# Kernel optimization log

Measured on AMD Instinct MI355X. Metric: run time of the kernel, lower is better.

## Reference

```python
import jax, jax.numpy as jnp
import numpy as np

NEAR, FAR, N_SAMPLES = 1.0, 6.0, 64
FAR_APPEND = 1000.0


def setup_inputs() -> dict:
    key = jax.random.key(0)
    ks = jax.random.split(key, 8)
    B, R = 2, 4096
    # pixel coords in a 128x128 image
    x_pix = jax.random.uniform(ks[0], (B, R, 2), dtype=jnp.float32) * 128.0
    # plausible pinhole intrinsics (fx=fy=128, cx=cy=64)
    K = jnp.array([[128.0, 0.0, 64.0], [0.0, 128.0, 64.0], [0.0, 0.0, 1.0]], dtype=jnp.float32)
    intrinsics = jnp.tile(K[None], (B, 1, 1))
    # identity rotation, small translation cam2world
    c2w = jnp.eye(4, dtype=jnp.float32).at[:3, 3].set(jnp.array([0.1, -0.2, 0.5]))
    cam2world = jnp.tile(c2w[None], (B, 1, 1))
    H = 256
    W1 = jax.random.normal(ks[1], (3, H), dtype=jnp.float32) / np.sqrt(3.0)
    b1 = jnp.zeros((H,), jnp.float32)
    W2 = jax.random.normal(ks[2], (H, H), dtype=jnp.float32) / np.sqrt(H)
    b2 = jnp.zeros((H,), jnp.float32)
    W3 = jax.random.normal(ks[3], (H, 4), dtype=jnp.float32) / np.sqrt(H)
    b3 = jnp.zeros((4,), jnp.float32)
    return {"x_pix": x_pix, "intrinsics": intrinsics, "cam2world": cam2world,
            "W1": W1, "b1": b1, "W2": W2, "b2": b2, "W3": W3, "b3": b3}


def _radiance_field(pts, W1, b1, W2, b2, W3, b3):
    # pts: (B, N, 3) -> sigma (B, N, 1), rad (B, N, 3)
    h = jax.nn.relu(pts @ W1 + b1)
    h = jax.nn.relu(h @ W2 + b2)
    o = h @ W3 + b3
    return jax.nn.relu(o[..., :1]), jax.nn.sigmoid(o[..., 1:])


def _get_world_rays(x_pix, intrinsics, cam2world):
    B, R, _ = x_pix.shape
    inv_K = jnp.linalg.inv(intrinsics)  # (B,3,3)
    xy_hom = jnp.concatenate([x_pix, jnp.ones((B, R, 1), x_pix.dtype)], axis=-1)  # (B,R,3)
    dirs_cam = jnp.einsum("bij,brj->bri", inv_K, xy_hom)  # unnormalized cam-frame dirs
    dirs_hom = jnp.concatenate([dirs_cam, jnp.zeros((B, R, 1), x_pix.dtype)], axis=-1)  # w=0 vector
    dirs_world = jnp.einsum("bij,brj->bri", cam2world, dirs_hom)[..., :3]
    origins = jnp.broadcast_to(cam2world[:, None, :3, 3], (B, R, 3))
    return origins, dirs_world


def _volume_integral(z_vals, sigmas, radiances):
    # z_vals: (S,); sigmas: (B,R,S,1); radiances: (B,R,S,3)
    dists = jnp.diff(z_vals, append=jnp.array([FAR_APPEND], z_vals.dtype))  # (S,)
    alpha = 1.0 - jnp.exp(-sigmas * dists[None, None, :, None])  # (B,R,S,1)
    Ts = jnp.cumprod(1.0 - alpha, axis=2)  # inclusive cumprod, matching torch
    weights = alpha * Ts  # (B,R,S,1)
    rgb = jnp.sum(weights * radiances, axis=2)  # (B,R,3)
    depth_map = jnp.einsum("brsv,s->brv", weights, z_vals)  # (B,R,1)
    return rgb, depth_map, weights


def reference(x_pix, intrinsics, cam2world, W1, b1, W2, b2, W3, b3):
    B, R = x_pix.shape[0], x_pix.shape[1]
    ros, rds = _get_world_rays(x_pix, intrinsics, cam2world)
    z_vals = jnp.linspace(NEAR, FAR, N_SAMPLES, dtype=x_pix.dtype)  # (S,)
    pts = ros[:, :, None, :] + rds[:, :, None, :] * z_vals[None, None, :, None]  # (B,R,S,3)
    pts = pts.reshape(B, -1, 3)
    sigma, rad = _radiance_field(pts, W1, b1, W2, b2, W3, b3)
    sigma = sigma.reshape(B, R, N_SAMPLES, 1)
    rad = rad.reshape(B, R, N_SAMPLES, 3)
    rgb, depth_map, weights = _volume_integral(z_vals, sigma, rad)
    accum = jnp.sum(weights, axis=-2)  # (B,R,1)
    rgb = rgb + (1.0 - accum)  # white background
    return rgb, depth_map
```

## Files before the change

kernel.cpp:

```cpp
#include <hip/hip_runtime.h>

typedef unsigned short u16;
typedef _Float16 f16x8 __attribute__((ext_vector_type(8)));
typedef float    f32x4  __attribute__((ext_vector_type(4)));
typedef float    f32x16 __attribute__((ext_vector_type(16)));

#define NRAYS 8192

#define WS_W2T  0
#define WS_B2   131072
#define WS_W3   132096
#define WS_B3   136192
#define WS_W1   136208
#define WS_B1   139280
#define WS_INTR 140304
#define WS_C2W  140384

__device__ __forceinline__ float bf2f(u16 u){
  union { unsigned int i; float f; } v; v.i = ((unsigned int)u) << 16; return v.f;
}
__device__ __forceinline__ u16 f2h(float f){
  union { _Float16 h; u16 u; } v; v.h = (_Float16)f;
  return v.u;
}
__device__ __forceinline__ int detect_bf16(const void* intr){
  return (((const u16*)intr)[0] == 0x4300u) ? 1 : 0;
}

__device__ __forceinline__ void conv_arr(const void* src, float* dst, int n, int bf, int tid){
  if (bf){
    const u16* s = (const u16*)src;
    for (int i = tid; i < n; i += 256) dst[i] = bf2f(s[i]);
  } else {
    const float* s = (const float*)src;
    for (int i = tid; i < n; i += 256) dst[i] = s[i];
  }
}

__global__ void prep(const void* __restrict__ W2, const void* __restrict__ W1,
                     const void* __restrict__ b1, const void* __restrict__ b2,
                     const void* __restrict__ W3, const void* __restrict__ b3,
                     const void* __restrict__ intr, const void* __restrict__ c2w,
                     char* __restrict__ ws)
{
  const int bf = detect_bf16(intr);
  const int t = threadIdx.x;
  if (blockIdx.x == 64){
    conv_arr(W1,  (float*)(ws + WS_W1),  768,  bf, t);
    conv_arr(b1,  (float*)(ws + WS_B1),  256,  bf, t);
    conv_arr(b2,  (float*)(ws + WS_B2),  256,  bf, t);
    conv_arr(W3,  (float*)(ws + WS_W3),  1024, bf, t);
    conv_arr(b3,  (float*)(ws + WS_B3),  4,    bf, t);
    conv_arr(intr,(float*)(ws + WS_INTR),18,   bf, t);
    conv_arr(c2w, (float*)(ws + WS_C2W), 32,   bf, t);
    return;
  }
  __shared__ u16 tile[32][34];
  const int bx = blockIdx.x & 7;
  const int by = blockIdx.x >> 3;
  const int c = t & 31, r = t >> 5;
  u16* W2T = (u16*)(ws + WS_W2T);
  #pragma unroll
  for (int rr = 0; rr < 32; rr += 8){
    int k = bx*32 + rr + r;
    int n = by*32 + c;
    float v = bf ? bf2f(((const u16*)W2)[k*256 + n]) : ((const float*)W2)[k*256 + n];
    tile[rr + r][c] = f2h(v);
  }
  __syncthreads();
  #pragma unroll
  for (int rr = 0; rr < 32; rr += 8){
    int n = by*32 + rr + r;
    int k = bx*32 + c;
    W2T[n*256 + k] = tile[c][rr + r];
  }
}

__device__ __forceinline__ void do_tail(const float* ob, int mrow, int rg, int l,
                                        f32x4 b3v, float* __restrict__ out)
{
  const float step = 5.0f / 63.0f;
  const f32x4* ob4 = (const f32x4*)ob;
  f32x4 oj = ob4[mrow] + ob4[128 + mrow] + ob4[256 + mrow] + ob4[384 + mrow];
  float o_s0 = oj.x + b3v.x;
  float o_s1 = oj.y + b3v.y;
  float o_s2 = oj.z + b3v.z;
  float o_s3 = oj.w + b3v.w;

  const float zc    = 1.0f + step * (float)l;
  const float znext = (l == 63) ? 1000.0f : (1.0f + step * (float)(l + 1));
  const float dist  = znext - zc;
  float sigma = fmaxf(o_s0, 0.0f);
  float alpha = 1.0f - __expf(-sigma * dist);
  float t = 1.0f - alpha;
  #pragma unroll
  for (int sh = 1; sh < 64; sh <<= 1){
    float u = __shfl_up(t, sh, 64);
    if (l >= sh) t *= u;
  }
  float wgt = alpha * t;
  float q0 = 1.0f / (1.0f + __expf(-o_s1));
  float q1 = 1.0f / (1.0f + __expf(-o_s2));
  float q2 = 1.0f / (1.0f + __expf(-o_s3));
  float s0 = wgt*q0, s1 = wgt*q1, s2 = wgt*q2, sw = wgt, sz = wgt*zc;
  #pragma unroll
  for (int sh = 1; sh < 64; sh <<= 1){
    s0 += __shfl_xor(s0, sh, 64);
    s1 += __shfl_xor(s1, sh, 64);
    s2 += __shfl_xor(s2, sh, 64);
    sw += __shfl_xor(sw, sh, 64);
    sz += __shfl_xor(sz, sh, 64);
  }
  if (l == 0){
    float bg = 1.0f - sw;
    out[rg*3 + 0] = s0 + bg;
    out[rg*3 + 1] = s1 + bg;
    out[rg*3 + 2] = s2 + bg;
    out[3*NRAYS + rg] = sz;
  }
}

__global__ __launch_bounds__(512, 4) void nerf_fused(
    const void* __restrict__ x_pix,
    const void* __restrict__ intr,
    const char* __restrict__ ws,
    float* __restrict__ out)
{
  __shared__ __align__(16) u16   h1s[128 * 256];
  __shared__ __align__(16) float obuf[4 * 128 * 4];
  __shared__ __align__(16) float cbuf[1280];

  const int tid = threadIdx.x;
  const int l   = tid & 63;
  const int w   = tid >> 6;
  const int rr  = w >> 2;
  const int ks  = w & 3;
  const int bf  = detect_bf16(intr);
  const int ray0g = blockIdx.x * 2;
  const int rayg  = ray0g + rr;
  const int bb    = ray0g >> 12;

  const float* intrf = (const float*)(ws + WS_INTR);
  const float* c2wf  = (const float*)(ws + WS_C2W);
  const float* W1f   = (const float*)(ws + WS_W1);
  const float* b1f   = (const float*)(ws + WS_B1);
  const float* b2f   = (const float*)(ws + WS_B2);
  const float* W3f   = (const float*)(ws + WS_W3);
  const u16*   W2T   = (const u16*)(ws + WS_W2T);

  if (tid < 256) cbuf[tid] = b2f[tid];
  cbuf[256 + tid]       = W3f[tid];
  cbuf[256 + 512 + tid] = W3f[512 + tid];

  float Ka[9], Mm[16];
  #pragma unroll
  for (int i = 0; i < 9;  i++) Ka[i] = intrf[bb*9  + i];
  #pragma unroll
  for (int i = 0; i < 16; i++) Mm[i] = c2wf[bb*16 + i];
  float a = Ka[0], b_ = Ka[1], c = Ka[2];
  float d = Ka[3], e  = Ka[4], f = Ka[5];
  float g = Ka[6], h_ = Ka[7], i9 = Ka[8];
  float det = a*(e*i9 - f*h_) - b_*(d*i9 - f*g) + c*(d*h_ - e*g);
  float inv = 1.0f / det;
  float i00 = (e*i9 - f*h_)*inv, i01 = (c*h_ - b_*i9)*inv, i02 = (b_*f - c*e)*inv;
  float i10 = (f*g - d*i9)*inv, i11 = (a*i9 - c*g)*inv, i12 = (c*d - a*f)*inv;
  float i20 = (d*h_ - e*g)*inv, i21 = (b_*g - a*h_)*inv, i22 = (a*e - b_*d)*inv;
  float ox = Mm[3], oy = Mm[7], oz = Mm[11];

  const int kbase = ks*64 + (l & 31)*2;
  const float2 w1r0 = *(const float2*)(W1f + kbase);
  const float2 w1r1 = *(const float2*)(W1f + 256 + kbase);
  const float2 w1r2 = *(const float2*)(W1f + 512 + kbase);
  const float2 w1bb = *(const float2*)(b1f + kbase);
  const float aa0 = ox*w1r0.x + oy*w1r1.x + oz*w1r2.x + w1bb.x;
  const float aa1 = ox*w1r0.y + oy*w1r1.y + oz*w1r2.y + w1bb.y;

  float px, py;
  if (bf){
    px = bf2f(((const u16*)x_pix)[rayg*2 + 0]);
    py = bf2f(((const u16*)x_pix)[rayg*2 + 1]);
  } else {
    px = ((const float*)x_pix)[rayg*2 + 0];
    py = ((const float*)x_pix)[rayg*2 + 1];
  }
  float gg0, gg1;
  {
    float dcx = i00*px + i01*py + i02;
    float dcy = i10*px + i11*py + i12;
    float dcz = i20*px + i21*py + i22;
    float dx = Mm[0]*dcx + Mm[1]*dcy + Mm[2]*dcz;
    float dy = Mm[4]*dcx + Mm[5]*dcy + Mm[6]*dcz;
    float dz = Mm[8]*dcx + Mm[9]*dcy + Mm[10]*dcz;
    gg0 = dx*w1r0.x + dy*w1r1.x + dz*w1r2.x;
    gg1 = dx*w1r0.y + dy*w1r1.y + dz*w1r2.y;
  }

  const float step = 5.0f / 63.0f;
  const int chunk_w = ks*8 + ((l & 31) >> 2);
  const int sub_b   = (l & 3) << 2;
  int off8[8];
  #pragma unroll
  for (int j = 0; j < 8; j++) off8[j] = ((chunk_w ^ j) << 4) + sub_b;

  const int l31 = l & 31;
  const int h   = l >> 5;
  const int m7  = l31 & 7;
  const int nbase = w * 32;
  const u16* Arow = W2T + (nbase + l31)*256 + h*8;
  const f32x4 b3v = *(const f32x4*)(ws + WS_B3);
  const char* hP = (const char*)h1s;

  {
    char* hb = (char*)h1s + (rr*64)*512;
    const int shalf = (l >> 5)*32;
    #pragma unroll 8
    for (int s2 = 0; s2 < 32; s2++){
      const int s = shalf + s2;
      float z = 1.0f + step * (float)s;
      u16 e0 = f2h(fmaxf(fmaf(gg0, z, aa0), 0.0f));
      u16 e1 = f2h(fmaxf(fmaf(gg1, z, aa1), 0.0f));
      *(unsigned*)(hb + s*512 + off8[s & 7]) = (unsigned)e0 | ((unsigned)e1 << 16);
    }
  }

  f16x8 ap[2];
  ap[0] = *(const f16x8*)(Arow);
  ap[1] = *(const f16x8*)(Arow + 16);

  __syncthreads();

  f32x16 acc[4];
  #pragma unroll
  for (int mt = 0; mt < 4; mt++)
    acc[mt] = (f32x16){0.f,0.f,0.f,0.f,0.f,0.f,0.f,0.f,
                       0.f,0.f,0.f,0.f,0.f,0.f,0.f,0.f};

  #pragma unroll
  for (int t = 0; t < 16; t++){
    f16x8 a0 = ap[t & 1];
    if (t + 2 < 16)
      ap[t & 1] = *(const f16x8*)(Arow + (t+2)*16);
    const int swz = ((2*t + h) ^ m7) << 4;
    f16x8 bfr[4];
    #pragma unroll
    for (int mt = 0; mt < 4; mt++)
      bfr[mt] = *(const f16x8*)(hP + (mt*32 + l31)*512 + swz);
    #pragma unroll
    for (int mt = 0; mt < 4; mt++)
      acc[mt] = __builtin_amdgcn_mfma_f32_32x32x16_f16(a0, bfr[mt], acc[mt], 0, 0, 0);
  }

  f32x4 o_m[4];
  #pragma unroll
  for (int mt = 0; mt < 4; mt++) o_m[mt] = (f32x4){0.f,0.f,0.f,0.f};
  #pragma unroll
  for (int gq = 0; gq < 4; gq++){
    const int n0 = nbase + gq*8 + h*4;
    f32x4 b2v = *(const f32x4*)(cbuf + n0);
    f32x4 w30 = *(const f32x4*)(cbuf + 256 + n0*4);
    f32x4 w31 = *(const f32x4*)(cbuf + 256 + (n0+1)*4);
    f32x4 w32 = *(const f32x4*)(cbuf + 256 + (n0+2)*4);
    f32x4 w33 = *(const f32x4*)(cbuf + 256 + (n0+3)*4);
    #pragma unroll
    for (int mt = 0; mt < 4; mt++){
      float h0 = fmaxf(acc[mt][gq*4+0] + b2v.x, 0.0f);
      float h1 = fmaxf(acc[mt][gq*4+1] + b2v.y, 0.0f);
      float h2 = fmaxf(acc[mt][gq*4+2] + b2v.z, 0.0f);
      float h3 = fmaxf(acc[mt][gq*4+3] + b2v.w, 0.0f);
      o_m[mt] = o_m[mt] + h0*w30 + h1*w31 + h2*w32 + h3*w33;
    }
  }

  #pragma unroll
  for (int mt = 0; mt < 4; mt++)
    #pragma unroll
    for (int j = 0; j < 4; j++){
      float v = o_m[mt][j];
      v += __shfl_xor(v, 32, 64);
      o_m[mt][j] = v;
    }

  if (w < 4 && h == 0){
    #pragma unroll
    for (int mt = 0; mt < 4; mt++)
      *(f32x4*)&obuf[(w*128 + mt*32 + l31)*4] = o_m[mt];
  }
  __syncthreads();

  if (w >= 4 && h == 0){
    #pragma unroll
    for (int mt = 0; mt < 4; mt++){
      const int idx = ((w - 4)*128 + mt*32 + l31)*4;
      f32x4 v = *(const f32x4*)&obuf[idx];
      *(f32x4*)&obuf[idx] = v + o_m[mt];
    }
  }
  __syncthreads();

  if (w == 0) do_tail(obuf, l,      ray0g,     l, b3v, out);
  if (w == 4) do_tail(obuf, 64 + l, ray0g + 1, l, b3v, out);
}

extern "C" void kernel_launch(void* const* d_in, const int* in_sizes, int n_in,
                              void* d_out, int out_size, void* d_ws, size_t ws_size,
                              hipStream_t stream)
{
  const void* x_pix = d_in[0];
  const void* intr  = d_in[1];
  const void* c2w   = d_in[2];
  const void* W1    = d_in[3];
  const void* b1    = d_in[4];
  const void* W2    = d_in[5];
  const void* b2    = d_in[6];
  const void* W3    = d_in[7];
  const void* b3    = d_in[8];
  float* outp = (float*)d_out;
  char*  ws   = (char*)d_ws;

  hipLaunchKernelGGL(prep, dim3(65), dim3(256), 0, stream,
                     W2, W1, b1, b2, W3, b3, intr, c2w, ws);
  hipLaunchKernelGGL(nerf_fused, dim3(NRAYS/2), dim3(512), 0, stream,
                     x_pix, intr, ws, outp);
}
```

Before: 165.9 us.

## Retile second-layer MFMA into 2x2 per-wave blocks with B-fragment prefetch

Each wave now covers a 64-wide output-channel slice and a 64-row sample half, instead of a 32-wide slice across all 128 rows. Per k-step it loads two A fragments (W2T, from global) and two B fragments (h1, from LDS) for four MFMAs, instead of one A and four B. B fragments are also double-buffered one step ahead. The cross-wave partial reduction through obuf drops its read-modify-write pass and one __syncthreads, since each wave writes its own slot. This cuts LDS traffic per MFMA at the cost of twice the global weight loads and somewhat more live registers.

```diff
diff --git a/kernel.cpp b/kernel.cpp
--- a/kernel.cpp
+++ b/kernel.cpp
@@ -205,8 +205,10 @@
   const int l31 = l & 31;
   const int h   = l >> 5;
   const int m7  = l31 & 7;
-  const int nbase = w * 32;
-  const u16* Arow = W2T + (nbase + l31)*256 + h*8;
+  const int ns  = w >> 1;
+  const int mh  = w & 1;
+  const u16* Arow = W2T + (ns*64 + l31)*256 + h*8;
+  const int mrow0 = mh*64 + l31;
   const f32x4 b3v = *(const f32x4*)(ws + WS_B3);
   const char* hP = (const char*)h1s;
 
@@ -223,56 +225,77 @@
     }
   }
 
-  f16x8 ap[2];
-  ap[0] = *(const f16x8*)(Arow);
-  ap[1] = *(const f16x8*)(Arow + 16);
+  f16x8 ap[2][2];
+  ap[0][0] = *(const f16x8*)(Arow);
+  ap[0][1] = *(const f16x8*)(Arow + 32*256);
+  ap[1][0] = *(const f16x8*)(Arow + 16);
+  ap[1][1] = *(const f16x8*)(Arow + 32*256 + 16);
 
   __syncthreads();
 
-  f32x16 acc[4];
-  #pragma unroll
-  for (int mt = 0; mt < 4; mt++)
-    acc[mt] = (f32x16){0.f,0.f,0.f,0.f,0.f,0.f,0.f,0.f,
-                       0.f,0.f,0.f,0.f,0.f,0.f,0.f,0.f};
+  f32x16 acc[2][2];
+  #pragma unroll
+  for (int nt = 0; nt < 2; nt++)
+    #pragma unroll
+    for (int mt = 0; mt < 2; mt++)
+      acc[nt][mt] = (f32x16){0.f,0.f,0.f,0.f,0.f,0.f,0.f,0.f,
+                             0.f,0.f,0.f,0.f,0.f,0.f,0.f,0.f};
+
+  f16x8 bp[2][2];
+  {
+    const int swz0 = ((0 + h) ^ m7) << 4;
+    bp[0][0] = *(const f16x8*)(hP + mrow0*512 + swz0);
+    bp[0][1] = *(const f16x8*)(hP + (mrow0 + 32)*512 + swz0);
+    const int swz1 = ((2 + h) ^ m7) << 4;
+    bp[1][0] = *(const f16x8*)(hP + mrow0*512 + swz1);
+    bp[1][1] = *(const f16x8*)(hP + (mrow0 + 32)*512 + swz1);
+  }
 
   #pragma unroll
   for (int t = 0; t < 16; t++){
-    f16x8 a0 = ap[t & 1];
-    if (t + 2 < 16)
-      ap[t & 1] = *(const f16x8*)(Arow + (t+2)*16);
-    const int swz = ((2*t + h) ^ m7) << 4;
-    f16x8 bfr[4];
+    f16x8 a0 = ap[t & 1][0];
+    f16x8 a1 = ap[t & 1][1];
+    f16x8 b0 = bp[t & 1][0];
+    f16x8 b1 = bp[t & 1][1];
+    if (t + 2 < 16){
+      ap[t & 1][0] = *(const f16x8*)(Arow + (t+2)*16);
+      ap[t & 1][1] = *(const f16x8*)(Arow + 32*256 + (t+2)*16);
+      const int swzn = ((2*(t+2) + h) ^ m7) << 4;
+      bp[t & 1][0] = *(const f16x8*)(hP + mrow0*512 + swzn);
+      bp[t & 1][1] = *(const f16x8*)(hP + (mrow0 + 32)*512 + swzn);
+    }
+    acc[0][0] = __builtin_amdgcn_mfma_f32_32x32x16_f16(a0, b0, acc[0][0], 0, 0, 0);
+    acc[1][0] = __builtin_amdgcn_mfma_f32_32x32x16_f16(a1, b0, acc[1][0], 0, 0, 0);
+    acc[0][1] = __builtin_amdgcn_mfma_f32_32x32x16_f16(a0, b1, acc[0][1], 0, 0, 0);
+    acc[1][1] = __builtin_amdgcn_mfma_f32_32x32x16_f16(a1, b1, acc[1][1], 0, 0, 0);
+  }
+
+  f32x4 o_m[2];
+  o_m[0] = (f32x4){0.f,0.f,0.f,0.f};
+  o_m[1] = (f32x4){0.f,0.f,0.f,0.f};
+  #pragma unroll
+  for (int nt = 0; nt < 2; nt++){
     #pragma unroll
-    for (int mt = 0; mt < 4; mt++)
-      bfr[mt] = *(const f16x8*)(hP + (mt*32 + l31)*512 + swz);
-    #pragma unroll
-    for (int mt = 0; mt < 4; mt++)
-      acc[mt] = __builtin_amdgcn_mfma_f32_32x32x16_f16(a0, bfr[mt], acc[mt], 0, 0, 0);
-  }
-
-  f32x4 o_m[4];
-  #pragma unroll
-  for (int mt = 0; mt < 4; mt++) o_m[mt] = (f32x4){0.f,0.f,0.f,0.f};
-  #pragma unroll
-  for (int gq = 0; gq < 4; gq++){
-    const int n0 = nbase + gq*8 + h*4;
-    f32x4 b2v = *(const f32x4*)(cbuf + n0);
-    f32x4 w30 = *(const f32x4*)(cbuf + 256 + n0*4);
-    f32x4 w31 = *(const f32x4*)(cbuf + 256 + (n0+1)*4);
-    f32x4 w32 = *(const f32x4*)(cbuf + 256 + (n0+2)*4);
-    f32x4 w33 = *(const f32x4*)(cbuf + 256 + (n0+3)*4);
-    #pragma unroll
-    for (int mt = 0; mt < 4; mt++){
-      float h0 = fmaxf(acc[mt][gq*4+0] + b2v.x, 0.0f);
-      float h1 = fmaxf(acc[mt][gq*4+1] + b2v.y, 0.0f);
-      float h2 = fmaxf(acc[mt][gq*4+2] + b2v.z, 0.0f);
-      float h3 = fmaxf(acc[mt][gq*4+3] + b2v.w, 0.0f);
-      o_m[mt] = o_m[mt] + h0*w30 + h1*w31 + h2*w32 + h3*w33;
+    for (int gq = 0; gq < 4; gq++){
+      const int n0 = ns*64 + nt*32 + gq*8 + h*4;
+      f32x4 b2v = *(const f32x4*)(cbuf + n0);
+      f32x4 w30 = *(const f32x4*)(cbuf + 256 + n0*4);
+      f32x4 w31 = *(const f32x4*)(cbuf + 256 + (n0+1)*4);
+      f32x4 w32 = *(const f32x4*)(cbuf + 256 + (n0+2)*4);
+      f32x4 w33 = *(const f32x4*)(cbuf + 256 + (n0+3)*4);
+      #pragma unroll
+      for (int mt = 0; mt < 2; mt++){
+        float h0 = fmaxf(acc[nt][mt][gq*4+0] + b2v.x, 0.0f);
+        float h1 = fmaxf(acc[nt][mt][gq*4+1] + b2v.y, 0.0f);
+        float h2 = fmaxf(acc[nt][mt][gq*4+2] + b2v.z, 0.0f);
+        float h3 = fmaxf(acc[nt][mt][gq*4+3] + b2v.w, 0.0f);
+        o_m[mt] = o_m[mt] + h0*w30 + h1*w31 + h2*w32 + h3*w33;
+      }
     }
   }
 
   #pragma unroll
-  for (int mt = 0; mt < 4; mt++)
+  for (int mt = 0; mt < 2; mt++)
     #pragma unroll
     for (int j = 0; j < 4; j++){
       float v = o_m[mt][j];
@@ -280,20 +303,10 @@
       o_m[mt][j] = v;
     }
 
-  if (w < 4 && h == 0){
+  if (h == 0){
     #pragma unroll
-    for (int mt = 0; mt < 4; mt++)
-      *(f32x4*)&obuf[(w*128 + mt*32 + l31)*4] = o_m[mt];
-  }
-  __syncthreads();
-
-  if (w >= 4 && h == 0){
-    #pragma unroll
-    for (int mt = 0; mt < 4; mt++){
-      const int idx = ((w - 4)*128 + mt*32 + l31)*4;
-      f32x4 v = *(const f32x4*)&obuf[idx];
-      *(f32x4*)&obuf[idx] = v + o_m[mt];
-    }
+    for (int mt = 0; mt < 2; mt++)
+      *(f32x4*)&obuf[(ns*128 + mh*64 + mt*32 + l31)*4] = o_m[mt];
   }
   __syncthreads();
 
```

Measured after the change: 211.7 us. +27.6%, slower.
